# Performance work log

Hardware: AMD Instinct MI355X
Metric: run time of the kernel (lower is better)

## Reference

```python
import jax, jax.numpy as jnp
import numpy as np

BS, K, DIM = 16384, 1000, 768
GAMMA = 1.0


def setup_inputs() -> dict:
    key = jax.random.key(0)
    k1, k2, k3 = jax.random.split(key, 3)
    # one-hot mask selecting one semantic dipole per sample
    idx = jax.random.randint(k1, (BS,), 0, K)
    support_sets_mask = jax.nn.one_hot(idx, K, dtype=jnp.float32)
    # z: points on the unit sphere S^{dim-1}
    z = jax.random.normal(k2, (BS, DIM), dtype=jnp.float32)
    z = z / jnp.linalg.norm(z, axis=1, keepdims=True)
    # SUPPORT_SETS = semantic_dipoles_features reshaped to [K, 2*dim] (unit CLIP features per pole)
    sdf = jax.random.normal(k3, (K, 2, DIM), dtype=jnp.float32)
    sdf = sdf / jnp.linalg.norm(sdf, axis=2, keepdims=True)
    SUPPORT_SETS = sdf.reshape(K, 2 * DIM)
    # ALPHAS[k] = [1, -1]; LOGGAMMA = log(gamma) * ones
    ALPHAS = jnp.tile(jnp.array([1.0, -1.0], dtype=jnp.float32), (K, 1))
    LOGGAMMA = jnp.full((K, 2), np.log(GAMMA), dtype=jnp.float32)
    return {"support_sets_mask": support_sets_mask, "z": z,
            "SUPPORT_SETS": SUPPORT_SETS, "ALPHAS": ALPHAS, "LOGGAMMA": LOGGAMMA}


def reference(support_sets_mask, z, SUPPORT_SETS, ALPHAS, LOGGAMMA):
    bs, dim = z.shape
    # select dipole params per sample via mask matmuls
    support_sets_batch = (support_sets_mask @ SUPPORT_SETS).reshape(bs, 2, dim)  # [bs,2,dim]
    alphas_batch = (support_sets_mask @ ALPHAS)[:, :, None]                      # [bs,2,1]
    gammas_batch = jnp.exp(support_sets_mask @ LOGGAMMA)[:, :, None]             # [bs,2,1]
    # RBF gradient field: grad_f = -2 * sum_j alpha_j * gamma_j * exp(-gamma_j ||z - s_j||^2) * (z - s_j)
    D = z[:, None, :] - support_sets_batch                                       # [bs,2,dim]
    sq_norm = jnp.sum(D * D, axis=2, keepdims=True)                              # [bs,2,1]
    grad_f = -2.0 * jnp.sum(alphas_batch * gammas_batch * jnp.exp(-gammas_batch * sq_norm) * D, axis=1)  # [bs,dim]
    # tangent-space projection onto T_z S^{n}: (I - z z^T) w == w - (z.w) z  (rank-1 form)
    proj = grad_f - jnp.sum(z * grad_f, axis=1, keepdims=True) * z
    # normalize
    return proj / jnp.linalg.norm(proj, axis=1, keepdims=True)
```

## Files before the change

kernel.cpp:

```cpp
#include <hip/hip_runtime.h>


constexpr int K   = 1000;
constexpr int DIM = 768;

__global__ __launch_bounds__(256) void css_kernel(
    const float* __restrict__ mask,
    const float* __restrict__ z,
    const float* __restrict__ ss,
    const float* __restrict__ alphas,
    const float* __restrict__ loggamma,
    float* __restrict__ out,
    int bs)
{
    const int gid  = blockIdx.x * blockDim.x + threadIdx.x;
    const int b    = gid >> 6;
    const int lane = threadIdx.x & 63;
    if (b >= bs) return;

    const float4* mrow = (const float4*)(mask + (size_t)b * K);
    int found = -1;
    #pragma unroll
    for (int i = 0; i < 4; ++i) {
        int e = lane + i * 64;
        if (e < 250) {
            float4 v = mrow[e];
            if (v.x != 0.f) found = e * 4 + 0;
            if (v.y != 0.f) found = e * 4 + 1;
            if (v.z != 0.f) found = e * 4 + 2;
            if (v.w != 0.f) found = e * 4 + 3;
        }
    }

    const float4* zrow = (const float4*)(z + (size_t)b * DIM);
    float4 z4[3];
    #pragma unroll
    for (int i = 0; i < 3; ++i) z4[i] = zrow[lane + i * 64];

    #pragma unroll
    for (int off = 1; off < 64; off <<= 1)
        found = max(found, __shfl_xor(found, off, 64));
    const int k = (found < 0) ? 0 : found;

    const float4* srow = (const float4*)(ss + (size_t)k * (2 * DIM));
    float4 d0[3], d1[3];
    float sqn0 = 0.f, sqn1 = 0.f;
    #pragma unroll
    for (int i = 0; i < 3; ++i) {
        float4 s0 = srow[lane + i * 64];
        float4 s1 = srow[192 + lane + i * 64];
        d0[i].x = z4[i].x - s0.x;  d0[i].y = z4[i].y - s0.y;
        d0[i].z = z4[i].z - s0.z;  d0[i].w = z4[i].w - s0.w;
        d1[i].x = z4[i].x - s1.x;  d1[i].y = z4[i].y - s1.y;
        d1[i].z = z4[i].z - s1.z;  d1[i].w = z4[i].w - s1.w;
        sqn0 += d0[i].x*d0[i].x + d0[i].y*d0[i].y + d0[i].z*d0[i].z + d0[i].w*d0[i].w;
        sqn1 += d1[i].x*d1[i].x + d1[i].y*d1[i].y + d1[i].z*d1[i].z + d1[i].w*d1[i].w;
    }
    #pragma unroll
    for (int off = 1; off < 64; off <<= 1) {
        sqn0 += __shfl_xor(sqn0, off, 64);
        sqn1 += __shfl_xor(sqn1, off, 64);
    }

    const float a0 = alphas[2 * k];
    const float a1 = alphas[2 * k + 1];
    const float g0 = expf(loggamma[2 * k]);
    const float g1 = expf(loggamma[2 * k + 1]);
    const float c0 = -2.f * a0 * g0 * expf(-g0 * sqn0);
    const float c1 = -2.f * a1 * g1 * expf(-g1 * sqn1);

    float4 g[3];
    float dot = 0.f;
    #pragma unroll
    for (int i = 0; i < 3; ++i) {
        g[i].x = c0 * d0[i].x + c1 * d1[i].x;
        g[i].y = c0 * d0[i].y + c1 * d1[i].y;
        g[i].z = c0 * d0[i].z + c1 * d1[i].z;
        g[i].w = c0 * d0[i].w + c1 * d1[i].w;
        dot += z4[i].x*g[i].x + z4[i].y*g[i].y + z4[i].z*g[i].z + z4[i].w*g[i].w;
    }
    #pragma unroll
    for (int off = 1; off < 64; off <<= 1) dot += __shfl_xor(dot, off, 64);

    float nsq = 0.f;
    #pragma unroll
    for (int i = 0; i < 3; ++i) {
        g[i].x -= dot * z4[i].x;
        g[i].y -= dot * z4[i].y;
        g[i].z -= dot * z4[i].z;
        g[i].w -= dot * z4[i].w;
        nsq += g[i].x*g[i].x + g[i].y*g[i].y + g[i].z*g[i].z + g[i].w*g[i].w;
    }
    #pragma unroll
    for (int off = 1; off < 64; off <<= 1) nsq += __shfl_xor(nsq, off, 64);

    const float inv = 1.f / sqrtf(nsq);
    float4* orow = (float4*)(out + (size_t)b * DIM);
    #pragma unroll
    for (int i = 0; i < 3; ++i) {
        float4 r;
        r.x = g[i].x * inv; r.y = g[i].y * inv;
        r.z = g[i].z * inv; r.w = g[i].w * inv;
        orow[lane + i * 64] = r;
    }
}

extern "C" void kernel_launch(void* const* d_in, const int* in_sizes, int n_in,
                              void* d_out, int out_size, void* d_ws, size_t ws_size,
                              hipStream_t stream) {
    const float* mask     = (const float*)d_in[0];
    const float* z        = (const float*)d_in[1];
    const float* ss       = (const float*)d_in[2];
    const float* alphas   = (const float*)d_in[3];
    const float* loggamma = (const float*)d_in[4];
    float* out = (float*)d_out;

    const int bs = in_sizes[1] / DIM;
    const int waves_per_block = 256 / 64;
    const int grid = (bs + waves_per_block - 1) / waves_per_block;
    css_kernel<<<grid, 256, 0, stream>>>(mask, z, ss, alphas, loggamma, out, bs);
}
```

Baseline: 162.2 us.

## Split mask index search into separate kernel and collapse reductions algebraically

Moves the one-hot mask scan into a dedicated grid-stride kernel that writes one index per sample to workspace. The main kernel then reads that index, loads z and the support rows together, and computes all needed dot products in a single fused butterfly reduction. The norm of the projected gradient is derived algebraically from those dot products, which removes the two extra dependent wave reductions. The cost is a second kernel launch and a workspace round trip, and the index is no longer initialized, so it depends on every row having a nonzero entry. The expanded norm formula may also be less precise numerically.

```diff
diff --git a/kernel.cpp b/kernel.cpp
--- a/kernel.cpp
+++ b/kernel.cpp
@@ -3,9 +3,26 @@
 
 constexpr int K   = 1000;
 constexpr int DIM = 768;
+constexpr int VPR = K / 4;
 
-__global__ __launch_bounds__(256) void css_kernel(
-    const float* __restrict__ mask,
+__global__ __launch_bounds__(256) void css_idx_kernel(
+    const float4* __restrict__ mask4, int* __restrict__ idx, int nvec)
+{
+    int i = blockIdx.x * blockDim.x + threadIdx.x;
+    const int stride = gridDim.x * blockDim.x;
+    for (; i < nvec; i += stride) {
+        float4 v = mask4[i];
+        if (v.x != 0.f || v.y != 0.f || v.z != 0.f || v.w != 0.f) {
+            int b = i / VPR;
+            int j = (i - b * VPR) * 4;
+            int c = (v.x != 0.f) ? 0 : (v.y != 0.f) ? 1 : (v.z != 0.f) ? 2 : 3;
+            idx[b] = j + c;
+        }
+    }
+}
+
+__global__ __launch_bounds__(256) void css_main_kernel(
+    const int*   __restrict__ idx,
     const float* __restrict__ z,
     const float* __restrict__ ss,
     const float* __restrict__ alphas,
@@ -18,35 +35,22 @@
     const int lane = threadIdx.x & 63;
     if (b >= bs) return;
 
-    const float4* mrow = (const float4*)(mask + (size_t)b * K);
-    int found = -1;
-    #pragma unroll
-    for (int i = 0; i < 4; ++i) {
-        int e = lane + i * 64;
-        if (e < 250) {
-            float4 v = mrow[e];
-            if (v.x != 0.f) found = e * 4 + 0;
-            if (v.y != 0.f) found = e * 4 + 1;
-            if (v.z != 0.f) found = e * 4 + 2;
-            if (v.w != 0.f) found = e * 4 + 3;
-        }
-    }
+    int k = idx[b];
+    k = (k < 0) ? 0 : (k >= K ? K - 1 : k);
+
+    const float a0 = alphas[2 * k];
+    const float a1 = alphas[2 * k + 1];
+    const float lg0 = loggamma[2 * k];
+    const float lg1 = loggamma[2 * k + 1];
 
     const float4* zrow = (const float4*)(z + (size_t)b * DIM);
-    float4 z4[3];
-    #pragma unroll
-    for (int i = 0; i < 3; ++i) z4[i] = zrow[lane + i * 64];
+    const float4* srow = (const float4*)(ss + (size_t)k * (2 * DIM));
 
-    #pragma unroll
-    for (int off = 1; off < 64; off <<= 1)
-        found = max(found, __shfl_xor(found, off, 64));
-    const int k = (found < 0) ? 0 : found;
-
-    const float4* srow = (const float4*)(ss + (size_t)k * (2 * DIM));
-    float4 d0[3], d1[3];
-    float sqn0 = 0.f, sqn1 = 0.f;
+    float4 z4[3], d0[3], d1[3];
+    float sqn0 = 0.f, sqn1 = 0.f, zd0 = 0.f, zd1 = 0.f, d01 = 0.f, zsq = 0.f;
     #pragma unroll
     for (int i = 0; i < 3; ++i) {
+        z4[i] = zrow[lane + i * 64];
         float4 s0 = srow[lane + i * 64];
         float4 s1 = srow[192 + lane + i * 64];
         d0[i].x = z4[i].x - s0.x;  d0[i].y = z4[i].y - s0.y;
@@ -55,52 +59,38 @@
         d1[i].z = z4[i].z - s1.z;  d1[i].w = z4[i].w - s1.w;
         sqn0 += d0[i].x*d0[i].x + d0[i].y*d0[i].y + d0[i].z*d0[i].z + d0[i].w*d0[i].w;
         sqn1 += d1[i].x*d1[i].x + d1[i].y*d1[i].y + d1[i].z*d1[i].z + d1[i].w*d1[i].w;
+        zd0  += z4[i].x*d0[i].x + z4[i].y*d0[i].y + z4[i].z*d0[i].z + z4[i].w*d0[i].w;
+        zd1  += z4[i].x*d1[i].x + z4[i].y*d1[i].y + z4[i].z*d1[i].z + z4[i].w*d1[i].w;
+        d01  += d0[i].x*d1[i].x + d0[i].y*d1[i].y + d0[i].z*d1[i].z + d0[i].w*d1[i].w;
+        zsq  += z4[i].x*z4[i].x + z4[i].y*z4[i].y + z4[i].z*z4[i].z + z4[i].w*z4[i].w;
     }
     #pragma unroll
     for (int off = 1; off < 64; off <<= 1) {
         sqn0 += __shfl_xor(sqn0, off, 64);
         sqn1 += __shfl_xor(sqn1, off, 64);
+        zd0  += __shfl_xor(zd0,  off, 64);
+        zd1  += __shfl_xor(zd1,  off, 64);
+        d01  += __shfl_xor(d01,  off, 64);
+        zsq  += __shfl_xor(zsq,  off, 64);
     }
 
-    const float a0 = alphas[2 * k];
-    const float a1 = alphas[2 * k + 1];
-    const float g0 = expf(loggamma[2 * k]);
-    const float g1 = expf(loggamma[2 * k + 1]);
+    const float g0 = expf(lg0);
+    const float g1 = expf(lg1);
     const float c0 = -2.f * a0 * g0 * expf(-g0 * sqn0);
     const float c1 = -2.f * a1 * g1 * expf(-g1 * sqn1);
+    const float dot    = c0 * zd0 + c1 * zd1;
+    const float gradsq = c0*c0*sqn0 + 2.f*c0*c1*d01 + c1*c1*sqn1;
+    const float nsq    = gradsq - 2.f*dot*dot + dot*dot*zsq;
+    const float inv    = 1.f / sqrtf(nsq);
 
-    float4 g[3];
-    float dot = 0.f;
-    #pragma unroll
-    for (int i = 0; i < 3; ++i) {
-        g[i].x = c0 * d0[i].x + c1 * d1[i].x;
-        g[i].y = c0 * d0[i].y + c1 * d1[i].y;
-        g[i].z = c0 * d0[i].z + c1 * d1[i].z;
-        g[i].w = c0 * d0[i].w + c1 * d1[i].w;
-        dot += z4[i].x*g[i].x + z4[i].y*g[i].y + z4[i].z*g[i].z + z4[i].w*g[i].w;
-    }
-    #pragma unroll
-    for (int off = 1; off < 64; off <<= 1) dot += __shfl_xor(dot, off, 64);
-
-    float nsq = 0.f;
-    #pragma unroll
-    for (int i = 0; i < 3; ++i) {
-        g[i].x -= dot * z4[i].x;
-        g[i].y -= dot * z4[i].y;
-        g[i].z -= dot * z4[i].z;
-        g[i].w -= dot * z4[i].w;
-        nsq += g[i].x*g[i].x + g[i].y*g[i].y + g[i].z*g[i].z + g[i].w*g[i].w;
-    }
-    #pragma unroll
-    for (int off = 1; off < 64; off <<= 1) nsq += __shfl_xor(nsq, off, 64);
-
-    const float inv = 1.f / sqrtf(nsq);
     float4* orow = (float4*)(out + (size_t)b * DIM);
     #pragma unroll
     for (int i = 0; i < 3; ++i) {
         float4 r;
-        r.x = g[i].x * inv; r.y = g[i].y * inv;
-        r.z = g[i].z * inv; r.w = g[i].w * inv;
+        r.x = (c0*d0[i].x + c1*d1[i].x - dot*z4[i].x) * inv;
+        r.y = (c0*d0[i].y + c1*d1[i].y - dot*z4[i].y) * inv;
+        r.z = (c0*d0[i].z + c1*d1[i].z - dot*z4[i].z) * inv;
+        r.w = (c0*d0[i].w + c1*d1[i].w - dot*z4[i].w) * inv;
         orow[lane + i * 64] = r;
     }
 }
@@ -114,9 +104,14 @@
     const float* alphas   = (const float*)d_in[3];
     const float* loggamma = (const float*)d_in[4];
     float* out = (float*)d_out;
+    int*   idx = (int*)d_ws;
 
-    const int bs = in_sizes[1] / DIM;
-    const int waves_per_block = 256 / 64;
-    const int grid = (bs + waves_per_block - 1) / waves_per_block;
-    css_kernel<<<grid, 256, 0, stream>>>(mask, z, ss, alphas, loggamma, out, bs);
+    const int bs   = in_sizes[1] / DIM;
+    const int nvec = bs * VPR;
+
+    const int k1_blocks = (nvec + 256 * 4 - 1) / (256 * 4);
+    css_idx_kernel<<<k1_blocks, 256, 0, stream>>>((const float4*)mask, idx, nvec);
+
+    const int k2_blocks = (bs + 3) / 4;
+    css_main_kernel<<<k2_blocks, 256, 0, stream>>>(idx, z, ss, alphas, loggamma, out, bs);
 }
```

Result: no change. 163.4 us (+0.8%).
